# Kernel tuning notes

Hardware: AMD Instinct MI355X
Metric: run time of the kernel (lower is better)

## Reference

```python
import jax, jax.numpy as jnp
import numpy as np

B, T, E, H = 4, 4096, 1024, 64

def setup_inputs() -> dict:
    key = jax.random.key(0)
    k1, k2, k3, k4 = jax.random.split(key, 4)
    embeddings = jax.random.normal(k1, (B, T, E), dtype=jnp.float32)
    Wq = jax.random.normal(k2, (H, E), dtype=jnp.float32) * (1.0 / np.sqrt(E))
    Wk = jax.random.normal(k3, (H, E), dtype=jnp.float32) * (1.0 / np.sqrt(E))
    Wv = jax.random.normal(k4, (H, E), dtype=jnp.float32) * (1.0 / np.sqrt(E))
    return {"embeddings": embeddings, "Wq": Wq, "Wk": Wk, "Wv": Wv}

def reference(embeddings, Wq, Wk, Wv):
    # Linear(E, H, bias=False): x @ W.T, W: [H, E]
    q = jnp.einsum('bte,he->bth', embeddings, Wq)  # [B,T,H]
    k = jnp.einsum('bte,he->bth', embeddings, Wk)  # [B,T,H]
    v = jnp.einsum('bte,he->bth', embeddings, Wv)  # [B,T,H]
    scale = embeddings.shape[-1] ** -0.5  # NOTE: source scales by embed_size**-0.5
    wei = jnp.einsum('bqh,bkh->bqk', q, k) * scale  # [B,T,T]
    Tn = embeddings.shape[1]
    causal = jnp.tril(jnp.ones((Tn, Tn), dtype=bool))
    wei = jnp.where(causal[None, :, :], wei, -jnp.inf)
    wei = jax.nn.softmax(wei, axis=-1)
    return jnp.einsum('bqk,bkh->bqh', wei, v)  # [B,T,H]
```

## Files before the change

### kernel.cpp

```cpp
#include <hip/hip_runtime.h>
#include <math.h>
#include <stdint.h>

#define BN 4
#define TN 4096
#define EN 1024
#define HN 64
#define BT (BN*TN)

typedef __attribute__((ext_vector_type(8))) short   short8;
typedef __attribute__((ext_vector_type(4))) float   f32x4;
typedef __attribute__((ext_vector_type(4))) unsigned short us4;
typedef __attribute__((ext_vector_type(8))) unsigned short us8;

__device__ __forceinline__ unsigned short f2b(float f) {
    union { float f; uint32_t u; } v; v.f = f;
    uint32_t u = v.u;
    return (unsigned short)((u + 0x7FFFu + ((u >> 16) & 1u)) >> 16);
}

__device__ __forceinline__ float fexp2(float x) {
#if __has_builtin(__builtin_amdgcn_exp2f)
    return __builtin_amdgcn_exp2f(x);
#else
    return exp2f(x);
#endif
}

__global__ __launch_bounds__(256)
void wconv(const float* __restrict__ Wq, const float* __restrict__ Wk,
           const float* __restrict__ Wv, unsigned short* __restrict__ W16) {
    const int row = blockIdx.x;
    const int t = threadIdx.x;
    const float* src;
    float sc = 1.0f;
    if (row < 64)       { src = Wq + (size_t)row * EN; sc = 0.045084220f; }
    else if (row < 128) { src = Wk + (size_t)(row - 64) * EN; }
    else                { src = Wv + (size_t)(row - 128) * EN; }
    float4 v = *(const float4*)(src + t * 4);
    us4 p;
    p[0] = f2b(v.x * sc); p[1] = f2b(v.y * sc);
    p[2] = f2b(v.z * sc); p[3] = f2b(v.w * sc);
    *(us4*)&W16[(size_t)row * EN + t * 4] = p;
}

__global__ __launch_bounds__(512, 2)
void qkv_gemm(const float* __restrict__ emb, const unsigned short* __restrict__ W16,
              unsigned short* __restrict__ QK, unsigned short* __restrict__ VT) {
    __shared__ __align__(16) unsigned short A_lds[2][64][72];
    __shared__ __align__(16) unsigned short B_lds[2][192][72];

    const int tid = threadIdx.x;
    const int wid = tid >> 6, lane = tid & 63;
    const int c = lane & 15, g = lane >> 4;
    const int wm = wid & 1, wn = wid >> 1;
    const int r0 = blockIdx.x * 64;
    const int ar = tid >> 3, ach = tid & 7;

    const int br0 = tid >> 3,           bch0 = tid & 7;
    const int br1 = (tid + 512) >> 3,   bch1 = bch0;
    const int br2 = (tid + 1024) >> 3,  bch2 = bch0;

    const f32x4 fzero = {0.f, 0.f, 0.f, 0.f};
    f32x4 acc[2][3];
    #pragma unroll
    for (int i = 0; i < 2; ++i)
        #pragma unroll
        for (int j = 0; j < 3; ++j) acc[i][j] = fzero;

    float4 pa0[2], pa1[2];
    us8 pb0[2], pb1[2], pb2[2];

    #pragma unroll
    for (int t = 0; t < 2; ++t) {
        const int k0 = t * 64;
        pa0[t] = *(const float4*)&emb[(size_t)(r0 + ar) * EN + k0 + ach * 8];
        pa1[t] = *(const float4*)&emb[(size_t)(r0 + ar) * EN + k0 + ach * 8 + 4];
        pb0[t] = *(const us8*)&W16[(size_t)br0 * EN + k0 + bch0 * 8];
        pb1[t] = *(const us8*)&W16[(size_t)br1 * EN + k0 + bch1 * 8];
        pb2[t] = *(const us8*)&W16[(size_t)br2 * EN + k0 + bch2 * 8];
    }
    {
        us8 ap;
        ap[0] = f2b(pa0[0].x); ap[1] = f2b(pa0[0].y); ap[2] = f2b(pa0[0].z); ap[3] = f2b(pa0[0].w);
        ap[4] = f2b(pa1[0].x); ap[5] = f2b(pa1[0].y); ap[6] = f2b(pa1[0].z); ap[7] = f2b(pa1[0].w);
        *(us8*)&A_lds[0][ar][ach * 8] = ap;
        *(us8*)&B_lds[0][br0][bch0 * 8] = pb0[0];
        *(us8*)&B_lds[0][br1][bch1 * 8] = pb1[0];
        *(us8*)&B_lds[0][br2][bch2 * 8] = pb2[0];
    }
    __syncthreads();

    #pragma unroll 2
    for (int t = 0; t < 16; ++t) {
        const int cur = t & 1;
        if (t + 2 < 16) {
            const int kn = (t + 2) * 64;
            pa0[cur] = *(const float4*)&emb[(size_t)(r0 + ar) * EN + kn + ach * 8];
            pa1[cur] = *(const float4*)&emb[(size_t)(r0 + ar) * EN + kn + ach * 8 + 4];
            pb0[cur] = *(const us8*)&W16[(size_t)br0 * EN + kn + bch0 * 8];
            pb1[cur] = *(const us8*)&W16[(size_t)br1 * EN + kn + bch1 * 8];
            pb2[cur] = *(const us8*)&W16[(size_t)br2 * EN + kn + bch2 * 8];
        }

        short8 af[2][2], bf[3][2];
        #pragma unroll
        for (int rt = 0; rt < 2; ++rt)
            #pragma unroll
            for (int ks = 0; ks < 2; ++ks)
                af[rt][ks] = *(const short8*)&A_lds[cur][32 * wm + 16 * rt + c][32 * ks + 8 * g];
        #pragma unroll
        for (int nt = 0; nt < 3; ++nt)
            #pragma unroll
            for (int ks = 0; ks < 2; ++ks)
                bf[nt][ks] = *(const short8*)&B_lds[cur][48 * wn + 16 * nt + c][32 * ks + 8 * g];
        #pragma unroll
        for (int ks = 0; ks < 2; ++ks)
            #pragma unroll
            for (int rt = 0; rt < 2; ++rt)
                #pragma unroll
                for (int nt = 0; nt < 3; ++nt)
                    acc[rt][nt] = __builtin_amdgcn_mfma_f32_16x16x32_bf16(
                        af[rt][ks], bf[nt][ks], acc[rt][nt], 0, 0, 0);

        if (t + 1 < 16) {
            const int nb = cur ^ 1;
            us8 ap;
            ap[0] = f2b(pa0[nb].x); ap[1] = f2b(pa0[nb].y); ap[2] = f2b(pa0[nb].z); ap[3] = f2b(pa0[nb].w);
            ap[4] = f2b(pa1[nb].x); ap[5] = f2b(pa1[nb].y); ap[6] = f2b(pa1[nb].z); ap[7] = f2b(pa1[nb].w);
            *(us8*)&A_lds[nb][ar][ach * 8] = ap;
            *(us8*)&B_lds[nb][br0][bch0 * 8] = pb0[nb];
            *(us8*)&B_lds[nb][br1][bch1 * 8] = pb1[nb];
            *(us8*)&B_lds[nb][br2][bch2 * 8] = pb2[nb];
        }
        __syncthreads();
    }

    #pragma unroll
    for (int rt = 0; rt < 2; ++rt) {
        #pragma unroll
        for (int nt = 0; nt < 3; ++nt) {
            const int n = 48 * wn + 16 * nt + c;
            const int wsel = n >> 6;
            const int d = n & 63;
            const int rbase = r0 + 32 * wm + 16 * rt + 4 * g;
            if (wsel < 2) {
                #pragma unroll
                for (int j = 0; j < 4; ++j)
                    QK[(size_t)wsel * BT * HN + (size_t)(rbase + j) * HN + d] =
                        f2b(acc[rt][nt][j]);
            } else {
                const int bb = rbase >> 12;
                const int tt = rbase & 4095;
                us4 p;
                #pragma unroll
                for (int j = 0; j < 4; ++j) p[j] = f2b(acc[rt][nt][j]);
                *(us4*)&VT[(size_t)bb * HN * TN + (size_t)d * TN + tt] = p;
            }
        }
    }
}

#define NW 8

__global__ __launch_bounds__(512, 4)
void attn(const unsigned short* __restrict__ QK,
          const unsigned short* __restrict__ VT, float* __restrict__ out) {
    __shared__ __align__(16) unsigned char SLAB[NW * 32 * 65 * 4];
    __shared__ __align__(16) float MLm[NW][32];
    __shared__ __align__(16) float MLl[NW][32];
    __shared__ __align__(16) float ML2m[32];
    __shared__ __align__(16) float ML2l[32];

    const int tid = threadIdx.x;
    const int w = tid >> 6, lane = tid & 63, c = lane & 15, g = lane >> 4;
    const int bid = blockIdx.x;
    const int b = bid & 3;
    const int qt = (TN / 32 - 1) - (bid >> 2);

    const unsigned short* Qg = QK + ((size_t)b * TN + (size_t)qt * 32) * HN;
    const unsigned short* Kg = QK + (size_t)BT * HN + (size_t)b * TN * HN;
    const unsigned short* Vg = VT + (size_t)b * HN * TN;

    unsigned short* Pw = (unsigned short*)SLAB + (size_t)w * 32 * 72;

    short8 bq[2][2];
    #pragma unroll
    for (int ct = 0; ct < 2; ++ct)
        #pragma unroll
        for (int ks = 0; ks < 2; ++ks)
            bq[ct][ks] = *(const short8*)&Qg[(size_t)(16 * ct + c) * HN + 32 * ks + 8 * g];

    const f32x4 fzero = {0.f, 0.f, 0.f, 0.f};
    f32x4 o[2][4];
    #pragma unroll
    for (int i = 0; i < 2; ++i)
        #pragma unroll
        for (int j = 0; j < 4; ++j) o[i][j] = fzero;
    float m[2] = {-INFINITY, -INFINITY};
    float l[2] = {0.f, 0.f};

    const int jmax = qt >> 1;

    for (int jt = w; jt <= jmax; jt += NW) {
        f32x4 st[4][2];
        #pragma unroll
        for (int kt = 0; kt < 4; ++kt)
            #pragma unroll
            for (int ct = 0; ct < 2; ++ct) st[kt][ct] = fzero;
        #pragma unroll
        for (int kt = 0; kt < 4; ++kt) {
            #pragma unroll
            for (int ks = 0; ks < 2; ++ks) {
                short8 ak = *(const short8*)
                    &Kg[((size_t)jt * 64 + 16 * kt + c) * HN + 32 * ks + 8 * g];
                #pragma unroll
                for (int ct = 0; ct < 2; ++ct)
                    st[kt][ct] = __builtin_amdgcn_mfma_f32_16x16x32_bf16(
                        ak, bq[ct][ks], st[kt][ct], 0, 0, 0);
            }
        }

        if (jt == jmax) {
            const int koff = jt * 64 - qt * 32;
            #pragma unroll
            for (int kt = 0; kt < 4; ++kt)
                #pragma unroll
                for (int ct = 0; ct < 2; ++ct)
                    #pragma unroll
                    for (int j = 0; j < 4; ++j)
                        if (16 * kt + 4 * g + j + koff > 16 * ct + c)
                            st[kt][ct][j] = -INFINITY;
        }

        #pragma unroll
        for (int ct = 0; ct < 2; ++ct) {
            float pmax = -INFINITY;
            #pragma unroll
            for (int kt = 0; kt < 4; ++kt)
                #pragma unroll
                for (int j = 0; j < 4; ++j) pmax = fmaxf(pmax, st[kt][ct][j]);
            pmax = fmaxf(pmax, __shfl_xor(pmax, 16));
            pmax = fmaxf(pmax, __shfl_xor(pmax, 32));
            const float mn = fmaxf(m[ct], pmax);
            const float alpha = fexp2(m[ct] - mn);
            float ls = 0.f;
            #pragma unroll
            for (int kt = 0; kt < 4; ++kt)
                #pragma unroll
                for (int j = 0; j < 4; ++j) {
                    float p = fexp2(st[kt][ct][j] - mn);
                    st[kt][ct][j] = p;
                    ls += p;
                }
            ls += __shfl_xor(ls, 16);
            ls += __shfl_xor(ls, 32);
            l[ct] = l[ct] * alpha + ls;
            m[ct] = mn;

            float a4[4];
            #pragma unroll
            for (int j = 0; j < 4; ++j) a4[j] = __shfl(alpha, 4 * g + j);
            #pragma unroll
            for (int dt = 0; dt < 4; ++dt)
                #pragma unroll
                for (int j = 0; j < 4; ++j) o[ct][dt][j] *= a4[j];
        }

        #pragma unroll
        for (int kt = 0; kt < 4; ++kt)
            #pragma unroll
            for (int ct = 0; ct < 2; ++ct) {
                us4 p;
                #pragma unroll
                for (int j = 0; j < 4; ++j) p[j] = f2b(st[kt][ct][j]);
                *(us4*)&Pw[(16 * ct + c) * 72 + 16 * kt + 4 * g] = p;
            }

        #pragma unroll
        for (int ks = 0; ks < 2; ++ks) {
            short8 pa[2];
            #pragma unroll
            for (int qp = 0; qp < 2; ++qp)
                pa[qp] = *(const short8*)&Pw[(16 * qp + c) * 72 + 32 * ks + 8 * g];
            #pragma unroll
            for (int dt = 0; dt < 4; ++dt) {
                short8 bv = *(const short8*)
                    &Vg[(size_t)(16 * dt + c) * TN + jt * 64 + 32 * ks + 8 * g];
                #pragma unroll
                for (int qp = 0; qp < 2; ++qp)
                    o[qp][dt] = __builtin_amdgcn_mfma_f32_16x16x32_bf16(
                        pa[qp], bv, o[qp][dt], 0, 0, 0);
            }
        }
    }

    if (g == 0) {
        MLm[w][c]      = m[0];  MLl[w][c]      = l[0];
        MLm[w][c + 16] = m[1];  MLl[w][c + 16] = l[1];
    }
    __syncthreads();

    if (tid < 32) {
        const int q = tid;
        float M = MLm[0][q];
        #pragma unroll
        for (int s = 1; s < NW; ++s) M = fmaxf(M, MLm[s][q]);
        float L = 0.f;
        #pragma unroll
        for (int s = 0; s < NW; ++s) L += MLl[s][q] * fexp2(MLm[s][q] - M);
        ML2m[q] = M;
        ML2l[q] = L;
    }
    __syncthreads();

    float* Oslab = (float*)SLAB;
    float* Ow = Oslab + (size_t)w * (32 * 65);
    #pragma unroll
    for (int qp = 0; qp < 2; ++qp) {
        float mo[4];
        #pragma unroll
        for (int j = 0; j < 4; ++j) mo[j] = __shfl(m[qp], 4 * g + j);
        #pragma unroll
        for (int j = 0; j < 4; ++j) {
            const int q = 16 * qp + 4 * g + j;
            const float sc = fexp2(mo[j] - ML2m[q]);
            #pragma unroll
            for (int dt = 0; dt < 4; ++dt)
                Ow[q * 65 + 16 * dt + c] = o[qp][dt][j] * sc;
        }
    }
    __syncthreads();

    const int d = 16 * (w & 3) + c;
    const int qb = 16 * (w >> 2);
    #pragma unroll
    for (int j = 0; j < 4; ++j) {
        const int q = qb + 4 * g + j;
        float v = 0.f;
        #pragma unroll
        for (int s = 0; s < NW; ++s) v += Oslab[(size_t)s * (32 * 65) + q * 65 + d];
        out[((size_t)b * TN + (size_t)qt * 32 + q) * HN + d] = v / ML2l[q];
    }
}

extern "C" void kernel_launch(void* const* d_in, const int* in_sizes, int n_in,
                              void* d_out, int out_size, void* d_ws, size_t ws_size,
                              hipStream_t stream) {
    const float* emb = (const float*)d_in[0];
    const float* Wq  = (const float*)d_in[1];
    const float* Wk  = (const float*)d_in[2];
    const float* Wv  = (const float*)d_in[3];
    float* out = (float*)d_out;

    unsigned short* ws  = (unsigned short*)d_ws;
    unsigned short* W16 = ws;
    unsigned short* QK  = ws + 196608;
    unsigned short* VT  = ws + 196608 + 2 * (size_t)BT * HN;

    wconv<<<192, 256, 0, stream>>>(Wq, Wk, Wv, W16);
    qkv_gemm<<<BT / 64, 512, 0, stream>>>(emb, W16, QK, VT);
    attn<<<BN * (TN / 32), 512, 0, stream>>>(QK, VT, out);
}
```

Measured before the change: 163.8 us.

## Stage K/V tiles through LDS with register prefetch; halve GEMM row tile and attention waves

```diff
diff --git a/kernel.cpp b/kernel.cpp
--- a/kernel.cpp
+++ b/kernel.cpp
@@ -47,26 +47,25 @@
 __global__ __launch_bounds__(512, 2)
 void qkv_gemm(const float* __restrict__ emb, const unsigned short* __restrict__ W16,
               unsigned short* __restrict__ QK, unsigned short* __restrict__ VT) {
-    __shared__ __align__(16) unsigned short A_lds[2][64][72];
+    __shared__ __align__(16) unsigned short A_lds[2][32][72];
     __shared__ __align__(16) unsigned short B_lds[2][192][72];
 
     const int tid = threadIdx.x;
     const int wid = tid >> 6, lane = tid & 63;
     const int c = lane & 15, g = lane >> 4;
     const int wm = wid & 1, wn = wid >> 1;
-    const int r0 = blockIdx.x * 64;
+    const int r0 = blockIdx.x * 32;
+
+    const bool doA = (tid < 256);
     const int ar = tid >> 3, ach = tid & 7;
-
     const int br0 = tid >> 3,           bch0 = tid & 7;
-    const int br1 = (tid + 512) >> 3,   bch1 = bch0;
-    const int br2 = (tid + 1024) >> 3,  bch2 = bch0;
+    const int br1 = (tid + 512) >> 3;
+    const int br2 = (tid + 1024) >> 3;
 
     const f32x4 fzero = {0.f, 0.f, 0.f, 0.f};
-    f32x4 acc[2][3];
-    #pragma unroll
-    for (int i = 0; i < 2; ++i)
-        #pragma unroll
-        for (int j = 0; j < 3; ++j) acc[i][j] = fzero;
+    f32x4 acc[3];
+    #pragma unroll
+    for (int j = 0; j < 3; ++j) acc[j] = fzero;
 
     float4 pa0[2], pa1[2];
     us8 pb0[2], pb1[2], pb2[2];
@@ -74,20 +73,24 @@
     #pragma unroll
     for (int t = 0; t < 2; ++t) {
         const int k0 = t * 64;
-        pa0[t] = *(const float4*)&emb[(size_t)(r0 + ar) * EN + k0 + ach * 8];
-        pa1[t] = *(const float4*)&emb[(size_t)(r0 + ar) * EN + k0 + ach * 8 + 4];
+        if (doA) {
+            pa0[t] = *(const float4*)&emb[(size_t)(r0 + ar) * EN + k0 + ach * 8];
+            pa1[t] = *(const float4*)&emb[(size_t)(r0 + ar) * EN + k0 + ach * 8 + 4];
+        }
         pb0[t] = *(const us8*)&W16[(size_t)br0 * EN + k0 + bch0 * 8];
-        pb1[t] = *(const us8*)&W16[(size_t)br1 * EN + k0 + bch1 * 8];
-        pb2[t] = *(const us8*)&W16[(size_t)br2 * EN + k0 + bch2 * 8];
+        pb1[t] = *(const us8*)&W16[(size_t)br1 * EN + k0 + bch0 * 8];
+        pb2[t] = *(const us8*)&W16[(size_t)br2 * EN + k0 + bch0 * 8];
     }
     {
-        us8 ap;
-        ap[0] = f2b(pa0[0].x); ap[1] = f2b(pa0[0].y); ap[2] = f2b(pa0[0].z); ap[3] = f2b(pa0[0].w);
-        ap[4] = f2b(pa1[0].x); ap[5] = f2b(pa1[0].y); ap[6] = f2b(pa1[0].z); ap[7] = f2b(pa1[0].w);
-        *(us8*)&A_lds[0][ar][ach * 8] = ap;
+        if (doA) {
+            us8 ap;
+            ap[0] = f2b(pa0[0].x); ap[1] = f2b(pa0[0].y); ap[2] = f2b(pa0[0].z); ap[3] = f2b(pa0[0].w);
+            ap[4] = f2b(pa1[0].x); ap[5] = f2b(pa1[0].y); ap[6] = f2b(pa1[0].z); ap[7] = f2b(pa1[0].w);
+            *(us8*)&A_lds[0][ar][ach * 8] = ap;
+        }
         *(us8*)&B_lds[0][br0][bch0 * 8] = pb0[0];
-        *(us8*)&B_lds[0][br1][bch1 * 8] = pb1[0];
-        *(us8*)&B_lds[0][br2][bch2 * 8] = pb2[0];
+        *(us8*)&B_lds[0][br1][bch0 * 8] = pb1[0];
+        *(us8*)&B_lds[0][br2][bch0 * 8] = pb2[0];
     }
     __syncthreads();
 
@@ -96,19 +99,19 @@
         const int cur = t & 1;
         if (t + 2 < 16) {
             const int kn = (t + 2) * 64;
-            pa0[cur] = *(const float4*)&emb[(size_t)(r0 + ar) * EN + kn + ach * 8];
-            pa1[cur] = *(const float4*)&emb[(size_t)(r0 + ar) * EN + kn + ach * 8 + 4];
+            if (doA) {
+                pa0[cur] = *(const float4*)&emb[(size_t)(r0 + ar) * EN + kn + ach * 8];
+                pa1[cur] = *(const float4*)&emb[(size_t)(r0 + ar) * EN + kn + ach * 8 + 4];
+            }
             pb0[cur] = *(const us8*)&W16[(size_t)br0 * EN + kn + bch0 * 8];
-            pb1[cur] = *(const us8*)&W16[(size_t)br1 * EN + kn + bch1 * 8];
-            pb2[cur] = *(const us8*)&W16[(size_t)br2 * EN + kn + bch2 * 8];
-        }
-
-        short8 af[2][2], bf[3][2];
-        #pragma unroll
-        for (int rt = 0; rt < 2; ++rt)
-            #pragma unroll
-            for (int ks = 0; ks < 2; ++ks)
-                af[rt][ks] = *(const short8*)&A_lds[cur][32 * wm + 16 * rt + c][32 * ks + 8 * g];
+            pb1[cur] = *(const us8*)&W16[(size_t)br1 * EN + kn + bch0 * 8];
+            pb2[cur] = *(const us8*)&W16[(size_t)br2 * EN + kn + bch0 * 8];
+        }
+
+        short8 af[2], bf[3][2];
+        #pragma unroll
+        for (int ks = 0; ks < 2; ++ks)
+            af[ks] = *(const short8*)&A_lds[cur][16 * wm + c][32 * ks + 8 * g];
         #pragma unroll
         for (int nt = 0; nt < 3; ++nt)
             #pragma unroll
@@ -117,56 +120,53 @@
         #pragma unroll
         for (int ks = 0; ks < 2; ++ks)
             #pragma unroll
-            for (int rt = 0; rt < 2; ++rt)
-                #pragma unroll
-                for (int nt = 0; nt < 3; ++nt)
-                    acc[rt][nt] = __builtin_amdgcn_mfma_f32_16x16x32_bf16(
-                        af[rt][ks], bf[nt][ks], acc[rt][nt], 0, 0, 0);
+            for (int nt = 0; nt < 3; ++nt)
+                acc[nt] = __builtin_amdgcn_mfma_f32_16x16x32_bf16(
+                    af[ks], bf[nt][ks], acc[nt], 0, 0, 0);
 
         if (t + 1 < 16) {
             const int nb = cur ^ 1;
-            us8 ap;
-            ap[0] = f2b(pa0[nb].x); ap[1] = f2b(pa0[nb].y); ap[2] = f2b(pa0[nb].z); ap[3] = f2b(pa0[nb].w);
-            ap[4] = f2b(pa1[nb].x); ap[5] = f2b(pa1[nb].y); ap[6] = f2b(pa1[nb].z); ap[7] = f2b(pa1[nb].w);
-            *(us8*)&A_lds[nb][ar][ach * 8] = ap;
+            if (doA) {
+                us8 ap;
+                ap[0] = f2b(pa0[nb].x); ap[1] = f2b(pa0[nb].y); ap[2] = f2b(pa0[nb].z); ap[3] = f2b(pa0[nb].w);
+                ap[4] = f2b(pa1[nb].x); ap[5] = f2b(pa1[nb].y); ap[6] = f2b(pa1[nb].z); ap[7] = f2b(pa1[nb].w);
+                *(us8*)&A_lds[nb][ar][ach * 8] = ap;
+            }
             *(us8*)&B_lds[nb][br0][bch0 * 8] = pb0[nb];
-            *(us8*)&B_lds[nb][br1][bch1 * 8] = pb1[nb];
-            *(us8*)&B_lds[nb][br2][bch2 * 8] = pb2[nb];
+            *(us8*)&B_lds[nb][br1][bch0 * 8] = pb1[nb];
+            *(us8*)&B_lds[nb][br2][bch0 * 8] = pb2[nb];
         }
         __syncthreads();
     }
 
     #pragma unroll
-    for (int rt = 0; rt < 2; ++rt) {
-        #pragma unroll
-        for (int nt = 0; nt < 3; ++nt) {
-            const int n = 48 * wn + 16 * nt + c;
-            const int wsel = n >> 6;
-            const int d = n & 63;
-            const int rbase = r0 + 32 * wm + 16 * rt + 4 * g;
-            if (wsel < 2) {
-                #pragma unroll
-                for (int j = 0; j < 4; ++j)
-                    QK[(size_t)wsel * BT * HN + (size_t)(rbase + j) * HN + d] =
-                        f2b(acc[rt][nt][j]);
-            } else {
-                const int bb = rbase >> 12;
-                const int tt = rbase & 4095;
-                us4 p;
-                #pragma unroll
-                for (int j = 0; j < 4; ++j) p[j] = f2b(acc[rt][nt][j]);
-                *(us4*)&VT[(size_t)bb * HN * TN + (size_t)d * TN + tt] = p;
-            }
-        }
-    }
-}
-
-#define NW 8
-
-__global__ __launch_bounds__(512, 4)
+    for (int nt = 0; nt < 3; ++nt) {
+        const int n = 48 * wn + 16 * nt + c;
+        const int wsel = n >> 6;
+        const int d = n & 63;
+        const int rbase = r0 + 16 * wm + 4 * g;
+        if (wsel < 2) {
+            #pragma unroll
+            for (int j = 0; j < 4; ++j)
+                QK[(size_t)wsel * BT * HN + (size_t)(rbase + j) * HN + d] =
+                    f2b(acc[nt][j]);
+        } else {
+            const int bb = rbase >> 12;
+            const int tt = rbase & 4095;
+            us4 p;
+            #pragma unroll
+            for (int j = 0; j < 4; ++j) p[j] = f2b(acc[nt][j]);
+            *(us4*)&VT[(size_t)bb * HN * TN + (size_t)d * TN + tt] = p;
+        }
+    }
+}
+
+#define NW 4
+
+__global__ __launch_bounds__(256, 2)
 void attn(const unsigned short* __restrict__ QK,
           const unsigned short* __restrict__ VT, float* __restrict__ out) {
-    __shared__ __align__(16) unsigned char SLAB[NW * 32 * 65 * 4];
+    __shared__ __align__(16) unsigned short KV[NW][2][64][72];
     __shared__ __align__(16) float MLm[NW][32];
     __shared__ __align__(16) float MLl[NW][32];
     __shared__ __align__(16) float ML2m[32];
@@ -182,7 +182,8 @@
     const unsigned short* Kg = QK + (size_t)BT * HN + (size_t)b * TN * HN;
     const unsigned short* Vg = VT + (size_t)b * HN * TN;
 
-    unsigned short* Pw = (unsigned short*)SLAB + (size_t)w * 32 * 72;
+    unsigned short* Ks = &KV[w][0][0][0];
+    unsigned short* Vs = &KV[w][1][0][0];
 
     short8 bq[2][2];
     #pragma unroll
@@ -201,8 +202,32 @@
     float l[2] = {0.f, 0.f};
 
     const int jmax = qt >> 1;
+    const int sr = lane >> 3, sc8 = lane & 7;
+
+    us8 kreg[8], vreg[8];
+    if (w <= jmax) {
+        #pragma unroll
+        for (int i = 0; i < 8; ++i) {
+            kreg[i] = *(const us8*)&Kg[((size_t)w * 64 + sr + 8 * i) * HN + sc8 * 8];
+            vreg[i] = *(const us8*)&Vg[(size_t)(sr + 8 * i) * TN + w * 64 + sc8 * 8];
+        }
+    }
 
     for (int jt = w; jt <= jmax; jt += NW) {
+        #pragma unroll
+        for (int i = 0; i < 8; ++i) {
+            *(us8*)&Ks[(sr + 8 * i) * 72 + sc8 * 8] = kreg[i];
+            *(us8*)&Vs[(sr + 8 * i) * 72 + sc8 * 8] = vreg[i];
+        }
+        if (jt + NW <= jmax) {
+            const int jn = jt + NW;
+            #pragma unroll
+            for (int i = 0; i < 8; ++i) {
+                kreg[i] = *(const us8*)&Kg[((size_t)jn * 64 + sr + 8 * i) * HN + sc8 * 8];
+                vreg[i] = *(const us8*)&Vg[(size_t)(sr + 8 * i) * TN + jn * 64 + sc8 * 8];
+            }
+        }
+
         f32x4 st[4][2];
         #pragma unroll
         for (int kt = 0; kt < 4; ++kt)
@@ -212,8 +237,7 @@
         for (int kt = 0; kt < 4; ++kt) {
             #pragma unroll
             for (int ks = 0; ks < 2; ++ks) {
-                short8 ak = *(const short8*)
-                    &Kg[((size_t)jt * 64 + 16 * kt + c) * HN + 32 * ks + 8 * g];
+                short8 ak = *(const short8*)&Ks[(16 * kt + c) * 72 + 32 * ks + 8 * g];
                 #pragma unroll
                 for (int ct = 0; ct < 2; ++ct)
                     st[kt][ct] = __builtin_amdgcn_mfma_f32_16x16x32_bf16(
@@ -274,7 +298,7 @@
                 us4 p;
                 #pragma unroll
                 for (int j = 0; j < 4; ++j) p[j] = f2b(st[kt][ct][j]);
-                *(us4*)&Pw[(16 * ct + c) * 72 + 16 * kt + 4 * g] = p;
+                *(us4*)&Ks[(16 * ct + c) * 72 + 16 * kt + 4 * g] = p;
             }
 
         #pragma unroll
@@ -282,11 +306,10 @@
             short8 pa[2];
             #pragma unroll
             for (int qp = 0; qp < 2; ++qp)
-                pa[qp] = *(const short8*)&Pw[(16 * qp + c) * 72 + 32 * ks + 8 * g];
+                pa[qp] = *(const short8*)&Ks[(16 * qp + c) * 72 + 32 * ks + 8 * g];
             #pragma unroll
             for (int dt = 0; dt < 4; ++dt) {
-                short8 bv = *(const short8*)
-                    &Vg[(size_t)(16 * dt + c) * TN + jt * 64 + 32 * ks + 8 * g];
+                short8 bv = *(const short8*)&Vs[(16 * dt + c) * 72 + 32 * ks + 8 * g];
                 #pragma unroll
                 for (int qp = 0; qp < 2; ++qp)
                     o[qp][dt] = __builtin_amdgcn_mfma_f32_16x16x32_bf16(
@@ -314,7 +337,7 @@
     }
     __syncthreads();
 
-    float* Oslab = (float*)SLAB;
+    float* Oslab = (float*)&KV[0][0][0][0];
     float* Ow = Oslab + (size_t)w * (32 * 65);
     #pragma unroll
     for (int qp = 0; qp < 2; ++qp) {
@@ -332,11 +355,10 @@
     }
     __syncthreads();
 
-    const int d = 16 * (w & 3) + c;
-    const int qb = 16 * (w >> 2);
-    #pragma unroll
-    for (int j = 0; j < 4; ++j) {
-        const int q = qb + 4 * g + j;
+    const int d = 16 * w + c;
+    #pragma unroll
+    for (int tq = 0; tq < 8; ++tq) {
+        const int q = 4 * tq + g;
         float v = 0.f;
         #pragma unroll
         for (int s = 0; s < NW; ++s) v += Oslab[(size_t)s * (32 * 65) + q * 65 + d];
@@ -359,6 +381,6 @@
     unsigned short* VT  = ws + 196608 + 2 * (size_t)BT * HN;
 
     wconv<<<192, 256, 0, stream>>>(Wq, Wk, Wv, W16);
-    qkv_gemm<<<BT / 64, 512, 0, stream>>>(emb, W16, QK, VT);
-    attn<<<BN * (TN / 32), 512, 0, stream>>>(QK, VT, out);
-}
+    qkv_gemm<<<BT / 32, 512, 0, stream>>>(emb, W16, QK, VT);
+    attn<<<BN * (TN / 32), 256, 0, stream>>>(QK, VT, out);
+}
```

Result: faster. 144.8 us (-11.6%).
